# Kernel tuning notes

Hardware: AMD Instinct MI355X
Metric: run time of the kernel (lower is better)

Reference implementation:

```python
import jax, jax.numpy as jnp
import numpy as np

TEMPERATURE = 0.1
NORMALIZED = True


def _l2norm(x, eps=1e-12):
    # matches F.normalize(p=2, dim=1)
    n = jnp.sqrt(jnp.sum(x * x, axis=1, keepdims=True))
    return x / jnp.maximum(n, eps)


def setup_inputs() -> dict:
    key = jax.random.key(0)
    k1, k2, k3, k4 = jax.random.split(key, 4)
    B, D = 4096, 256
    return {
        "hs": jax.random.normal(k1, (B, D), dtype=jnp.float32),
        "ht0": jax.random.normal(k2, (B, D), dtype=jnp.float32),
        "ht1": jax.random.normal(k3, (B, D), dtype=jnp.float32),
        "labels": jax.random.randint(k4, (B,), 0, 100, dtype=jnp.int64)
        if jax.config.jax_enable_x64 else jax.random.randint(k4, (B,), 0, 100, dtype=jnp.int32),
        "num_views": 2,
    }


def _per_teacher_loss(hs_n, ht_n, mask, logits_mask, batch_size, num_views):
    # features: [N, D] with N = 2B
    features = jnp.concatenate([hs_n, ht_n], axis=0)
    sim = jnp.matmul(features, features.T) / TEMPERATURE          # [N, N]
    exp_logits = jnp.exp(sim) * logits_mask                        # [N, N]
    log_prob = sim - jnp.log(jnp.sum(exp_logits, axis=1, keepdims=True))
    per_inst = -jnp.sum(mask * log_prob, axis=1) / jnp.sum(mask, axis=1)  # [N]
    if num_views > 1:
        per_inst = per_inst.reshape(batch_size, num_views).mean(axis=1)
    return per_inst.mean()


def reference(hs, ht0, ht1, labels, num_views):
    batch_size = labels.shape[0]
    hs = hs.reshape(batch_size, -1)
    ht_list = [ht0.reshape(batch_size, -1), ht1.reshape(batch_size, -1)]
    if NORMALIZED:
        hs = _l2norm(hs)
        ht_list = [_l2norm(ht) for ht in ht_list]

    labels2 = jnp.concatenate([labels, labels])                    # [N]
    mask = (labels2[:, None] == labels2[None, :]).astype(jnp.float32)
    N = 2 * batch_size
    logits_mask = 1.0 - jnp.eye(N, dtype=jnp.float32)              # zero diagonal
    mask = mask * logits_mask

    inter_loss = 0.0
    for ht in ht_list:
        inter_loss = inter_loss + _per_teacher_loss(
            hs, ht, mask, logits_mask, batch_size, num_views)
    return inter_loss / len(ht_list)
```

## Files before the change

kernel.cpp:

```cpp
#include <hip/hip_runtime.h>
#include <hip/hip_bf16.h>

#define B_SIZE 4096
#define D_SIZE 256
#define N_SIZE 8192
#define FSCALE 3.798282555f
#define LN2    0.69314718056f

typedef __attribute__((ext_vector_type(8))) short short8;
typedef __attribute__((ext_vector_type(4))) short short4v;
typedef __attribute__((ext_vector_type(4))) float floatx4;


__device__ __forceinline__ void async16(void* lds, const void* g) {
    __builtin_amdgcn_global_load_lds(
        (const __attribute__((address_space(1))) unsigned int*)g,
        (__attribute__((address_space(3))) unsigned int*)lds, 16, 0, 0);
}

__global__ void norm_kernel(const float* __restrict__ hs,
                            const float* __restrict__ ht0,
                            const float* __restrict__ ht1,
                            __hip_bfloat16* __restrict__ dst,
                            float* __restrict__ zero_region,
                            const int* __restrict__ labels,
                            int* __restrict__ cnt, int* __restrict__ offv,
                            int* __restrict__ idxS) {
    const int bid = blockIdx.x;
    const int tid = threadIdx.x;
    const int wv  = tid >> 6;
    const int l   = tid & 63;

    int gid = bid * 256 + tid;
    if (gid < 20482) zero_region[gid] = 0.0f;

    int wgid = bid * 4 + wv;
    for (int r = wgid; r < 3 * B_SIZE; r += 2048) {
        const float* src = (r < B_SIZE)     ? hs  + r * D_SIZE
                         : (r < 2 * B_SIZE) ? ht0 + (r - B_SIZE) * D_SIZE
                                            : ht1 + (r - 2 * B_SIZE) * D_SIZE;
        float4 v = *reinterpret_cast<const float4*>(src + l * 4);
        float ss = v.x * v.x + v.y * v.y + v.z * v.z + v.w * v.w;
#pragma unroll
        for (int off = 32; off > 0; off >>= 1) ss += __shfl_xor(ss, off);
        float sc = FSCALE / fmaxf(sqrtf(ss), 1e-12f);
        __hip_bfloat16 b0 = __float2bfloat16(v.x * sc);
        __hip_bfloat16 b1 = __float2bfloat16(v.y * sc);
        __hip_bfloat16 b2 = __float2bfloat16(v.z * sc);
        __hip_bfloat16 b3 = __float2bfloat16(v.w * sc);
        short4v o;
        o[0] = *reinterpret_cast<short*>(&b0);
        o[1] = *reinterpret_cast<short*>(&b1);
        o[2] = *reinterpret_cast<short*>(&b2);
        o[3] = *reinterpret_cast<short*>(&b3);
        *reinterpret_cast<short4v*>(
            reinterpret_cast<short*>(dst) + r * D_SIZE + l * 4) = o;
    }

    if (bid == 0) {
        __shared__ int h[128], o2[128], ctr[128];
        if (tid < 128) { h[tid] = 0; ctr[tid] = 0; }
        __syncthreads();
        for (int i = tid; i < B_SIZE; i += 256) atomicAdd(&h[labels[i] & 127], 1);
        __syncthreads();
        if (tid == 0) {
            int s = 0;
            for (int c = 0; c < 128; ++c) { o2[c] = s; s += h[c]; }
        }
        __syncthreads();
        for (int i = tid; i < B_SIZE; i += 256) {
            int lab = labels[i] & 127;
            int pos = o2[lab] + atomicAdd(&ctr[lab], 1);
            idxS[pos] = i;
        }
        if (tid < 128) { cnt[tid] = h[tid]; offv[tid] = o2[tid]; }
    }
}

__global__ __launch_bounds__(256, 2)
void simgvec_kernel(const __hip_bfloat16* __restrict__ featS,
                    const __hip_bfloat16* __restrict__ featT0,
                    const __hip_bfloat16* __restrict__ featT1,
                    float* __restrict__ Sarr,
                    const int* __restrict__ cnt,
                    const int* __restrict__ offv,
                    const int* __restrict__ idxS,
                    float* __restrict__ gAll) {
    __shared__ __align__(16) unsigned char sB[2][32768];

    const int bid = blockIdx.x;
    const int tid = threadIdx.x;

    if (bid >= 920) {
        const int gb  = bid - 920;
        const int c   = gb & 127;
        const int set = gb >> 7;
        const __hip_bfloat16* f = featS + set * B_SIZE * D_SIZE;
        int* sIdx = (int*)&sB[0][0];
        const int n = cnt[c], o = offv[c];
        float acc = 0.0f;
        for (int base = 0; base < n; base += 256) {
            int m = n - base; if (m > 256) m = 256;
            __syncthreads();
            if (tid < m) sIdx[tid] = idxS[o + base + tid];
            __syncthreads();
            for (int k = 0; k < m; ++k)
                acc += __bfloat162float(f[sIdx[k] * D_SIZE + tid]);
        }
        gAll[set * 32768 + c * 256 + tid] = acc;
        return;
    }

    const int pb  = (bid & 7) * 115 + (bid >> 3);
    const int t   = (pb >= 528) ? 1 : 0;
    const int p   = t ? (pb - 392) : pb;
    const __hip_bfloat16* featT = t ? featT1 : featT0;

    int R = (int)((sqrtf((float)(8 * p + 1)) - 1.0f) * 0.5f);
    while ((R + 1) * (R + 2) / 2 <= p) ++R;
    while (R * (R + 1) / 2 > p) --R;
    const int C = p - R * (R + 1) / 2;

    const int w    = tid >> 6;
    const int l    = tid & 63;
    const int quad = l >> 4;
    const int lcol = l & 15;
    const int row_base = R * 256 + w * 64;

    float* tgt = (R < 16) ? (Sarr + 2 * N_SIZE) : (Sarr + t * N_SIZE);

    short8 af[4][8];
#pragma unroll
    for (int rt = 0; rt < 4; ++rt) {
        int arow = row_base + rt * 16 + lcol;
        const __hip_bfloat16* ap = (arow < B_SIZE) ? featS + arow * D_SIZE
                                                   : featT + (arow - B_SIZE) * D_SIZE;
#pragma unroll
        for (int ks = 0; ks < 8; ++ks)
            af[rt][ks] = *reinterpret_cast<const short8*>(ap + ks * 32 + quad * 8);
    }

    float Sp[4][4];
#pragma unroll
    for (int rt = 0; rt < 4; ++rt)
#pragma unroll
        for (int r = 0; r < 4; ++r) Sp[rt][r] = 0.0f;

    const int col0 = C * 256;

    auto stage = [&](int b, int cb) {
        int tb = cb + w * 16;
        const __hip_bfloat16* cp = (tb < B_SIZE) ? featS + tb * D_SIZE
                                                 : featT + (tb - B_SIZE) * D_SIZE;
        const char* gp = (const char*)cp + lcol * 512 + quad * 16;
        unsigned char* lp = &sB[b][w * 8192];
#pragma unroll
        for (int ks = 0; ks < 8; ++ks)
            async16(lp + ks * 1024, gp + ks * 64);
    };

    stage(0, col0);

    for (int g = 0; g < 4; ++g) {
        const int buf = g & 1;
        asm volatile("s_waitcnt vmcnt(0)" ::: "memory");
        __syncthreads();
        if (g + 1 < 4) stage(buf ^ 1, col0 + (g + 1) * 64);

        const int gcol = col0 + g * 64;
        if (gcol > row_base) continue;
        const bool diag = (gcol == row_base);

        float Cp[4] = {0.f, 0.f, 0.f, 0.f};
#pragma unroll
        for (int up = 0; up < 2; ++up) {
            floatx4 acc[2][4];
#pragma unroll
            for (int j = 0; j < 2; ++j)
#pragma unroll
                for (int rt = 0; rt < 4; ++rt) acc[j][rt] = floatx4{0.f, 0.f, 0.f, 0.f};

            __builtin_amdgcn_s_setprio(1);
#pragma unroll
            for (int ks = 0; ks < 8; ++ks) {
                short8 bf[2];
#pragma unroll
                for (int j = 0; j < 2; ++j)
                    bf[j] = *reinterpret_cast<const short8*>(
                        &sB[buf][(up * 2 + j) * 8192 + ks * 1024 + l * 16]);
#pragma unroll
                for (int j = 0; j < 2; ++j)
#pragma unroll
                    for (int rt = 0; rt < 4; ++rt)
                        acc[j][rt] = __builtin_amdgcn_mfma_f32_16x16x32_bf16(
                            af[rt][ks], bf[j], acc[j][rt], 0, 0, 0);
            }
            __builtin_amdgcn_s_setprio(0);
#pragma unroll
            for (int j = 0; j < 2; ++j)
#pragma unroll
                for (int rt = 0; rt < 4; ++rt)
#pragma unroll
                    for (int r = 0; r < 4; ++r) {
                        float e = exp2f(acc[j][rt][r]);
                        Sp[rt][r] += e;
                        Cp[up * 2 + j] += e;
                    }
        }

        if (!diag) {
#pragma unroll
            for (int u = 0; u < 4; ++u) {
                Cp[u] += __shfl_xor(Cp[u], 16);
                Cp[u] += __shfl_xor(Cp[u], 32);
            }
            if (quad == 0) {
#pragma unroll
                for (int u = 0; u < 4; ++u)
                    atomicAdd(&tgt[gcol + u * 16 + lcol], Cp[u]);
            }
        }
    }

#pragma unroll
    for (int rt = 0; rt < 4; ++rt)
#pragma unroll
        for (int r = 0; r < 4; ++r) {
#pragma unroll
            for (int m = 1; m < 16; m <<= 1) Sp[rt][r] += __shfl_xor(Sp[rt][r], m);
        }
    if (lcol == 0) {
#pragma unroll
        for (int rt = 0; rt < 4; ++rt)
#pragma unroll
            for (int r = 0; r < 4; ++r) {
                int row = row_base + rt * 16 + quad * 4 + r;
                atomicAdd(&tgt[row], Sp[rt][r]);
            }
    }
}

__global__ void rowstat_kernel(const __hip_bfloat16* __restrict__ featS,
                               const __hip_bfloat16* __restrict__ featT0,
                               const __hip_bfloat16* __restrict__ featT1,
                               const int* __restrict__ labels,
                               const float* __restrict__ gAll,
                               const int* __restrict__ cnt,
                               const float* __restrict__ Sarr,
                               float* __restrict__ lossAcc,
                               int* __restrict__ ticket,
                               float* __restrict__ out) {
    __shared__ float wpart[4];
    const float* SS = Sarr + 2 * N_SIZE;
    const int tid = threadIdx.x;
    const int wv  = tid >> 6;
    const int l   = tid & 63;
    const int waveid = blockIdx.x * 4 + wv;
    float psum = 0.0f;

    for (int it = 0; it < 8; ++it) {
        int R = waveid * 8 + it;
        int t = R >> 13;
        int i = R & (N_SIZE - 1);
        const __hip_bfloat16* f = (i < B_SIZE) ? featS + i * D_SIZE
                                : (t ? featT1 : featT0) + (i - B_SIZE) * D_SIZE;
        int lab = labels[i & (B_SIZE - 1)] & 127;
        short4v fb = *reinterpret_cast<const short4v*>(f + l * 4);
        float fx[4];
#pragma unroll
        for (int k = 0; k < 4; ++k) {
            unsigned int u = ((unsigned int)(unsigned short)fb[k]) << 16;
            fx[k] = __uint_as_float(u);
        }
        const float* gS = gAll + lab * 256 + l * 4;
        const float* gT = gAll + (1 + t) * 32768 + lab * 256 + l * 4;
        float dot = 0.f, aii = 0.f;
#pragma unroll
        for (int k = 0; k < 4; ++k) {
            dot += fx[k] * (gS[k] + gT[k]);
            aii += fx[k] * fx[k];
        }
#pragma unroll
        for (int m = 1; m < 64; m <<= 1) {
            dot += __shfl_xor(dot, m);
            aii += __shfl_xor(aii, m);
        }
        if (l == 0) {
            float S = Sarr[t * N_SIZE + i];
            if (i < B_SIZE) S += SS[i];
            float M = 2.0f * (float)cnt[lab] - 1.0f;
            float E = exp2f(aii);
            psum += logf(S - E) - LN2 * (dot - aii) / M;
        }
    }
    if (l == 0) wpart[wv] = psum;
    __syncthreads();
    if (tid == 0) {
        atomicAdd(lossAcc, wpart[0] + wpart[1] + wpart[2] + wpart[3]);
        __threadfence();
        if (atomicAdd(ticket, 1) == 511) {
            float tot = atomicAdd(lossAcc, 0.0f);
            out[0] = tot / 16384.0f;
        }
    }
}

extern "C" void kernel_launch(void* const* d_in, const int* in_sizes, int n_in,
                              void* d_out, int out_size, void* d_ws, size_t ws_size,
                              hipStream_t stream) {
    const float* hs     = (const float*)d_in[0];
    const float* ht0    = (const float*)d_in[1];
    const float* ht1    = (const float*)d_in[2];
    const int*   labels = (const int*)d_in[3];

    char* ws = (char*)d_ws;
    float* Sarr    = (float*)(ws);
    float* lossAcc = (float*)(ws + 81920);
    int*   ticket  = (int*)(ws + 81924);
    int*   cnt     = (int*)(ws + 82432);
    int*   offv    = (int*)(ws + 82944);
    int*   idxS    = (int*)(ws + 83456);
    float* gAll    = (float*)(ws + 99840);
    __hip_bfloat16* featS  = (__hip_bfloat16*)(ws + 524288);
    __hip_bfloat16* featT0 = (__hip_bfloat16*)(ws + 524288 + 2097152);
    __hip_bfloat16* featT1 = (__hip_bfloat16*)(ws + 524288 + 2 * 2097152);

    norm_kernel<<<512, 256, 0, stream>>>(hs, ht0, ht1, featS, (float*)ws,
                                         labels, cnt, offv, idxS);
    simgvec_kernel<<<1304, 256, 0, stream>>>(featS, featT0, featT1, Sarr,
                                             cnt, offv, idxS, gAll);
    rowstat_kernel<<<512, 256, 0, stream>>>(featS, featT0, featT1, labels, gAll, cnt,
                                            Sarr, lossAcc, ticket, (float*)d_out);
}
```

Baseline: 150.8 us.

## Single-buffer LDS and reload A fragments per half to raise occupancy

The similarity kernel moves from double-buffered to single-buffered LDS for the B tiles and stops holding all A fragments in registers. A fragments are now reloaded from global memory for each half of the row tiles at every column group. Launch bounds rise from 2 to 3 blocks per SIMD to exploit the smaller register and LDS footprint. In exchange, prefetch overlap is lost: staging now waits behind a barrier after compute, and A data is re-read from global/L2 repeatedly.

After: 187.2 us. 1.24x slower.

```diff
diff --git a/kernel.cpp b/kernel.cpp
--- a/kernel.cpp
+++ b/kernel.cpp
@@ -77,7 +77,7 @@
     }
 }
 
-__global__ __launch_bounds__(256, 2)
+__global__ __launch_bounds__(256, 3)
 void simgvec_kernel(const __hip_bfloat16* __restrict__ featS,
                     const __hip_bfloat16* __restrict__ featT0,
                     const __hip_bfloat16* __restrict__ featT1,
@@ -86,7 +86,7 @@
                     const int* __restrict__ offv,
                     const int* __restrict__ idxS,
                     float* __restrict__ gAll) {
-    __shared__ __align__(16) unsigned char sB[2][32768];
+    __shared__ __align__(16) unsigned char sB[32768];
 
     const int bid = blockIdx.x;
     const int tid = threadIdx.x;
@@ -96,7 +96,7 @@
         const int c   = gb & 127;
         const int set = gb >> 7;
         const __hip_bfloat16* f = featS + set * B_SIZE * D_SIZE;
-        int* sIdx = (int*)&sB[0][0];
+        int* sIdx = (int*)&sB[0];
         const int n = cnt[c], o = offv[c];
         float acc = 0.0f;
         for (int base = 0; base < n; base += 256) {
@@ -129,17 +129,6 @@
 
     float* tgt = (R < 16) ? (Sarr + 2 * N_SIZE) : (Sarr + t * N_SIZE);
 
-    short8 af[4][8];
-#pragma unroll
-    for (int rt = 0; rt < 4; ++rt) {
-        int arow = row_base + rt * 16 + lcol;
-        const __hip_bfloat16* ap = (arow < B_SIZE) ? featS + arow * D_SIZE
-                                                   : featT + (arow - B_SIZE) * D_SIZE;
-#pragma unroll
-        for (int ks = 0; ks < 8; ++ks)
-            af[rt][ks] = *reinterpret_cast<const short8*>(ap + ks * 32 + quad * 8);
-    }
-
     float Sp[4][4];
 #pragma unroll
     for (int rt = 0; rt < 4; ++rt)
@@ -148,77 +137,100 @@
 
     const int col0 = C * 256;
 
-    auto stage = [&](int b, int cb) {
+    auto stage = [&](int cb) {
         int tb = cb + w * 16;
         const __hip_bfloat16* cp = (tb < B_SIZE) ? featS + tb * D_SIZE
                                                  : featT + (tb - B_SIZE) * D_SIZE;
         const char* gp = (const char*)cp + lcol * 512 + quad * 16;
-        unsigned char* lp = &sB[b][w * 8192];
+        unsigned char* lp = &sB[w * 8192];
 #pragma unroll
         for (int ks = 0; ks < 8; ++ks)
             async16(lp + ks * 1024, gp + ks * 64);
     };
 
-    stage(0, col0);
+    stage(col0);
 
     for (int g = 0; g < 4; ++g) {
-        const int buf = g & 1;
         asm volatile("s_waitcnt vmcnt(0)" ::: "memory");
         __syncthreads();
-        if (g + 1 < 4) stage(buf ^ 1, col0 + (g + 1) * 64);
 
         const int gcol = col0 + g * 64;
-        if (gcol > row_base) continue;
-        const bool diag = (gcol == row_base);
-
-        float Cp[4] = {0.f, 0.f, 0.f, 0.f};
-#pragma unroll
-        for (int up = 0; up < 2; ++up) {
-            floatx4 acc[2][4];
-#pragma unroll
-            for (int j = 0; j < 2; ++j)
-#pragma unroll
-                for (int rt = 0; rt < 4; ++rt) acc[j][rt] = floatx4{0.f, 0.f, 0.f, 0.f};
-
-            __builtin_amdgcn_s_setprio(1);
-#pragma unroll
-            for (int ks = 0; ks < 8; ++ks) {
-                short8 bf[2];
-#pragma unroll
-                for (int j = 0; j < 2; ++j)
-                    bf[j] = *reinterpret_cast<const short8*>(
-                        &sB[buf][(up * 2 + j) * 8192 + ks * 1024 + l * 16]);
-#pragma unroll
-                for (int j = 0; j < 2; ++j)
-#pragma unroll
-                    for (int rt = 0; rt < 4; ++rt)
-                        acc[j][rt] = __builtin_amdgcn_mfma_f32_16x16x32_bf16(
-                            af[rt][ks], bf[j], acc[j][rt], 0, 0, 0);
+        if (gcol <= row_base) {
+            const bool diag = (gcol == row_base);
+
+            float Cp[4] = {0.f, 0.f, 0.f, 0.f};
+#pragma unroll
+            for (int h = 0; h < 2; ++h) {
+                short8 af[2][8];
+#pragma unroll
+                for (int rt2 = 0; rt2 < 2; ++rt2) {
+                    int arow = row_base + (2 * h + rt2) * 16 + lcol;
+                    const __hip_bfloat16* ap =
+                        (arow < B_SIZE) ? featS + arow * D_SIZE
+                                        : featT + (arow - B_SIZE) * D_SIZE;
+                    asm volatile("" : "+v"(ap));
+#pragma unroll
+                    for (int ks = 0; ks < 8; ++ks)
+                        af[rt2][ks] = *reinterpret_cast<const short8*>(
+                            ap + ks * 32 + quad * 8);
+                }
+
+#pragma unroll
+                for (int up = 0; up < 2; ++up) {
+                    floatx4 acc[2][2];
+#pragma unroll
+                    for (int j = 0; j < 2; ++j)
+#pragma unroll
+                        for (int rt2 = 0; rt2 < 2; ++rt2)
+                            acc[j][rt2] = floatx4{0.f, 0.f, 0.f, 0.f};
+
+                    __builtin_amdgcn_s_setprio(1);
+#pragma unroll
+                    for (int ks = 0; ks < 8; ++ks) {
+                        short8 bf[2];
+#pragma unroll
+                        for (int j = 0; j < 2; ++j)
+                            bf[j] = *reinterpret_cast<const short8*>(
+                                &sB[(up * 2 + j) * 8192 + ks * 1024 + l * 16]);
+#pragma unroll
+                        for (int j = 0; j < 2; ++j)
+#pragma unroll
+                            for (int rt2 = 0; rt2 < 2; ++rt2)
+                                acc[j][rt2] = __builtin_amdgcn_mfma_f32_16x16x32_bf16(
+                                    af[rt2][ks], bf[j], acc[j][rt2], 0, 0, 0);
+                    }
+                    __builtin_amdgcn_s_setprio(0);
+#pragma unroll
+                    for (int j = 0; j < 2; ++j)
+#pragma unroll
+                        for (int rt2 = 0; rt2 < 2; ++rt2)
+#pragma unroll
+                            for (int r = 0; r < 4; ++r) {
+                                float e = exp2f(acc[j][rt2][r]);
+                                Sp[2 * h + rt2][r] += e;
+                                Cp[up * 2 + j] += e;
+                            }
+                }
             }
-            __builtin_amdgcn_s_setprio(0);
-#pragma unroll
-            for (int j = 0; j < 2; ++j)
-#pragma unroll
-                for (int rt = 0; rt < 4; ++rt)
-#pragma unroll
-                    for (int r = 0; r < 4; ++r) {
-                        float e = exp2f(acc[j][rt][r]);
-                        Sp[rt][r] += e;
-                        Cp[up * 2 + j] += e;
-                    }
-        }
-
-        if (!diag) {
-#pragma unroll
-            for (int u = 0; u < 4; ++u) {
-                Cp[u] += __shfl_xor(Cp[u], 16);
-                Cp[u] += __shfl_xor(Cp[u], 32);
+
+            if (!diag) {
+#pragma unroll
+                for (int u = 0; u < 4; ++u) {
+                    Cp[u] += __shfl_xor(Cp[u], 16);
+                    Cp[u] += __shfl_xor(Cp[u], 32);
+                }
+                if (quad == 0) {
+#pragma unroll
+                    for (int u = 0; u < 4; ++u)
+                        atomicAdd(&tgt[gcol + u * 16 + lcol], Cp[u]);
+                }
             }
-            if (quad == 0) {
-#pragma unroll
-                for (int u = 0; u < 4; ++u)
-                    atomicAdd(&tgt[gcol + u * 16 + lcol], Cp[u]);
-            }
+        }
+
+        if (g + 1 < 4) {
+            asm volatile("s_waitcnt vmcnt(0) lgkmcnt(0)" ::: "memory");
+            __syncthreads();
+            stage(col0 + (g + 1) * 64);
         }
     }
 
```
